# Kernel optimization log

Measured on AMD Instinct MI355X. Metric: run time of the kernel, lower is better.

## Reference

```python
import jax, jax.numpy as jnp
import numpy as np
from jax import lax

# --- config (matches init_kwargs) ---
H = 1024          # hidden_size
I = 704           # moe_intermediate_size (per expert)
E = 32            # n_routed_experts
G = 8             # n_group
TOPK_GROUP = 3    # topk_group
K = 6             # num_experts_per_tok
N_SHARED = 2      # n_shared_experts -> shared intermediate = N_SHARED * I
SCALE = 1.0       # routed_scaling_factor
T = 2048          # number of tokens
CAP = 2 * (T * K) // E


def setup_inputs() -> dict:
    key = jax.random.key(0)
    ks = jax.random.split(key, 8)
    s = 0.02  # initializer_range
    Is = N_SHARED * I
    return {
        "x": jax.random.normal(ks[0], (T, H), jnp.float32),
        "gate_w": s * jax.random.normal(ks[1], (E, H), jnp.float32),   # router
        "w_gate": s * jax.random.normal(ks[2], (E, H, I), jnp.float32),
        "w_up":   s * jax.random.normal(ks[3], (E, H, I), jnp.float32),
        "w_down": s * jax.random.normal(ks[4], (E, I, H), jnp.float32),
        "sw_gate": s * jax.random.normal(ks[5], (H, Is), jnp.float32),
        "sw_up":   s * jax.random.normal(ks[6], (H, Is), jnp.float32),
        "sw_down": s * jax.random.normal(ks[7], (Is, H), jnp.float32),
    }


def _moe_forward(x, gate_w, w_gate, w_up, w_down, sw_gate, sw_up, sw_down):
    # ---- router: softmax scores + group-limited top-k (topk_method='gready') ----
    logits = x @ gate_w.T                                  # [T, E]
    scores = jax.nn.softmax(logits, axis=-1)               # [T, E]
    group_scores = scores.reshape(T, G, E // G).max(-1)    # [T, G]
    _, gidx = lax.top_k(group_scores, TOPK_GROUP)          # [T, topk_group]
    gmask = jnp.zeros((T, G), scores.dtype).at[jnp.arange(T)[:, None], gidx].set(1.0)
    emask = jnp.repeat(gmask, E // G, axis=1)              # [T, E]
    masked_scores = jnp.where(emask > 0, scores, 0.0)
    topk_w, topk_idx = lax.top_k(masked_scores, K)         # [T, K]
    # norm_topk_prob=False -> weights are raw softmax scores * routed_scaling_factor
    topk_w = topk_w * SCALE

    # ---- dispatch: sort assignments by expert, scatter into [E, CAP, H] buffers ----
    flat_e = topk_idx.reshape(-1)                          # [T*K]
    order = jnp.argsort(flat_e)
    se = flat_e[order]                                     # sorted expert ids
    tok = order // K                                       # source token of each slot
    counts = jax.ops.segment_sum(jnp.ones_like(flat_e), flat_e, num_segments=E)
    starts = jnp.cumsum(counts) - counts
    pos = jnp.arange(T * K) - starts[se]                   # position within expert
    valid = pos < CAP
    pos_w = jnp.where(valid, pos, CAP)                     # overflow slot CAP (sliced off)
    xbuf = jnp.zeros((E, CAP + 1, H), x.dtype).at[se, pos_w].set(x[tok])
    xb = xbuf[:, :CAP]                                     # [E, CAP, H]

    # ---- grouped expert MLPs: silu(x Wg) * (x Wu) @ Wd ----
    g = jnp.einsum("ech,ehi->eci", xb, w_gate)
    u = jnp.einsum("ech,ehi->eci", xb, w_up)
    yb = jnp.einsum("eci,eih->ech", jax.nn.silu(g) * u, w_down)  # [E, CAP, H]

    # ---- combine: gather back and weighted-scatter to tokens ----
    y_flat = yb[se, jnp.minimum(pos, CAP - 1)] * valid[:, None].astype(x.dtype)
    wts = topk_w.reshape(-1)[order]                        # [T*K]
    routed = jnp.zeros((T, H), x.dtype).at[tok].add(y_flat * wts[:, None])

    # ---- shared experts MLP (intermediate = n_shared * moe_inter) ----
    sg = jax.nn.silu(x @ sw_gate) * (x @ sw_up)
    shared = sg @ sw_down

    return routed + shared                                 # [T, H]


def reference(x, gate_w, w_gate, w_up, w_down, sw_gate, sw_up, sw_down):
    return _moe_forward(x, gate_w, w_gate, w_up, w_down, sw_gate, sw_up, sw_down)
```

## Files before the change

kernel.cpp:

```cpp
#include <hip/hip_runtime.h>
#include <hip/hip_bf16.h>

#define H 1024
#define I_DIM 704
#define E 32
#define TOPK_GROUP 3
#define K_TOP 6
#define T_TOK 2048
#define CAP 768
#define IS_DIM 1408
#define NCHUNK 192

typedef __attribute__((ext_vector_type(8))) short short8v;
typedef __attribute__((ext_vector_type(4))) float f32x4;

__device__ __forceinline__ unsigned short f2bfbits(float f) {
  unsigned u = __float_as_uint(f);
  unsigned r = (u + 0x7fffu + ((u >> 16) & 1u)) >> 16;
  return (unsigned short)r;
}
__device__ __forceinline__ float bf2f(unsigned short b) {
  return __uint_as_float(((unsigned)b) << 16);
}
__device__ __forceinline__ void gload_lds16(const short* g, short* l) {
  __builtin_amdgcn_global_load_lds(
      (const __attribute__((address_space(1))) unsigned int*)g,
      (__attribute__((address_space(3))) unsigned int*)l, 16, 0, 0);
}

__global__ void cast_x_kernel(const float* __restrict__ x, short* __restrict__ xb) {
  size_t i = ((size_t)blockIdx.x * 256 + threadIdx.x) * 4;
  float4 v = *(const float4*)(x + i);
  short4 s;
  s.x = (short)f2bfbits(v.x); s.y = (short)f2bfbits(v.y);
  s.z = (short)f2bfbits(v.z); s.w = (short)f2bfbits(v.w);
  *(short4*)(xb + i) = s;
}

__global__ __launch_bounds__(256) void tw_kernel(const float* __restrict__ in,
                                                 short* __restrict__ out,
                                                 int K, int N) {
  __shared__ float tile[64][65];
  long long eoff = (long long)blockIdx.z * (long long)K * N;
  const float* ip = in + eoff;
  short* op = out + eoff;
  int n0 = blockIdx.x * 64, k0 = blockIdx.y * 64;
  int t = threadIdx.x;
  int tr = t >> 4;
  int tc = (t & 15) * 4;
  #pragma unroll
  for (int i = 0; i < 4; ++i) {
    float4 v = *(const float4*)(ip + (size_t)(k0 + tr + i * 16) * N + n0 + tc);
    tile[tr + i * 16][tc + 0] = v.x;
    tile[tr + i * 16][tc + 1] = v.y;
    tile[tr + i * 16][tc + 2] = v.z;
    tile[tr + i * 16][tc + 3] = v.w;
  }
  __syncthreads();
  #pragma unroll
  for (int i = 0; i < 4; ++i) {
    int n = tr + i * 16;
    short4 s;
    s.x = (short)f2bfbits(tile[tc + 0][n]);
    s.y = (short)f2bfbits(tile[tc + 1][n]);
    s.z = (short)f2bfbits(tile[tc + 2][n]);
    s.w = (short)f2bfbits(tile[tc + 3][n]);
    *(short4*)(op + (size_t)(n0 + n) * K + k0 + tc) = s;
  }
}

__global__ __launch_bounds__(64) void gating_kernel(const float* __restrict__ x,
                                                    const float* __restrict__ gw,
                                                    int* __restrict__ tidx,
                                                    float* __restrict__ tw) {
  int t = blockIdx.x;
  int lane = threadIdx.x;
  int e = lane & 31, half = lane >> 5;
  const float4* xr4 = (const float4*)(x + (size_t)t * H + half * 512);
  const float4* wr4 = (const float4*)(gw + (size_t)e * H + half * 512);
  double acc = 0.0;
  #pragma unroll 4
  for (int j = 0; j < 128; ++j) {
    float4 a = xr4[j], b = wr4[j];
    acc += (double)a.x * b.x + (double)a.y * b.y + (double)a.z * b.z + (double)a.w * b.w;
  }
  acc += __shfl_down(acc, 32);
  double lg = acc;
  double m = lg;
  #pragma unroll
  for (int off = 16; off >= 1; off >>= 1) {
    double o = __shfl_xor(m, off);
    if (o > m) m = o;
  }
  double p = exp(lg - m);
  double sum = p;
  #pragma unroll
  for (int off = 16; off >= 1; off >>= 1) sum += __shfl_xor(sum, off);
  p /= sum;
  double gmax = p;
  { double o = __shfl_xor(gmax, 1); if (o > gmax) gmax = o;
    o = __shfl_xor(gmax, 2); if (o > gmax) gmax = o; }
  bool gsel = false;
  double gv = gmax;
  #pragma unroll
  for (int it = 0; it < TOPK_GROUP; ++it) {
    double v = gv; int gi = e >> 2;
    #pragma unroll
    for (int off = 16; off >= 1; off >>= 1) {
      double ov = __shfl_xor(v, off);
      int oi = __shfl_xor(gi, off);
      if (ov > v || (ov == v && oi < gi)) { v = ov; gi = oi; }
    }
    if ((e >> 2) == gi) { gsel = true; gv = -1e300; }
  }
  double mp = gsel ? p : 0.0;
  #pragma unroll
  for (int it = 0; it < K_TOP; ++it) {
    double v = mp; int ei = e;
    #pragma unroll
    for (int off = 16; off >= 1; off >>= 1) {
      double ov = __shfl_xor(v, off);
      int oi = __shfl_xor(ei, off);
      if (ov > v || (ov == v && oi < ei)) { v = ov; ei = oi; }
    }
    if (lane == 0) { tidx[t * K_TOP + it] = ei; tw[t * K_TOP + it] = (float)v; }
    if (e == ei) mp = -2.0;
  }
}

__global__ __launch_bounds__(64) void hist_kernel(const int* __restrict__ tidx,
                                                  int* __restrict__ chunk_hist) {
  __shared__ int h[E];
  int c = blockIdx.x, lane = threadIdx.x;
  if (lane < E) h[lane] = 0;
  __syncthreads();
  int te = tidx[c * 64 + lane];
  atomicAdd(&h[te], 1);
  __syncthreads();
  if (lane < E) chunk_hist[c * E + lane] = h[lane];
}

__global__ __launch_bounds__(1024) void scan_kernel(const int* __restrict__ chunk_hist,
                                                    int* __restrict__ chunk_base,
                                                    int* __restrict__ cnt) {
  __shared__ int h[NCHUNK * E];
  int t = threadIdx.x;
  for (int i = t; i < NCHUNK * E; i += 1024) h[i] = chunk_hist[i];
  __syncthreads();
  if (t < E) {
    int run = 0;
    for (int c = 0; c < NCHUNK; ++c) {
      int v = h[c * E + t];
      h[c * E + t] = run;
      run += v;
    }
    cnt[t] = run < CAP ? run : CAP;
  }
  __syncthreads();
  for (int i = t; i < NCHUNK * E; i += 1024) chunk_base[i] = h[i];
}

__global__ __launch_bounds__(64) void place_kernel(const int* __restrict__ tidx,
                                                   const int* __restrict__ chunk_base,
                                                   int* __restrict__ token_list,
                                                   int* __restrict__ sid) {
  int c = blockIdx.x, lane = threadIdx.x;
  int idx = c * 64 + lane;
  int te = tidx[idx];
  unsigned long long mymask = 0;
  #pragma unroll
  for (int e = 0; e < E; ++e) {
    unsigned long long bal = __ballot(te == e);
    if (te == e) mymask = bal;
  }
  int rank = __popcll(mymask & ((1ull << lane) - 1ull));
  int pos = chunk_base[c * E + te] + rank;
  int s = -1;
  if (pos < CAP) {
    token_list[te * CAP + pos] = idx / K_TOP;
    s = te * CAP + pos;
  }
  sid[idx] = s;
}

__global__ __launch_bounds__(256) void gateup_kernel(
    const short* __restrict__ Xb, const short* __restrict__ Wg, const short* __restrict__ Wu,
    short* __restrict__ Sout, const int* __restrict__ tlist, const int* __restrict__ cnt_dev,
    int Nld, long long wstride, long long sstride) {
  int e = blockIdx.z;
  int cnt = cnt_dev ? cnt_dev[e] : T_TOK;
  int row0 = blockIdx.y * 128;
  if (row0 >= cnt) return;
  int col0 = blockIdx.x * 64;
  const short* wg = Wg + (long long)e * wstride;
  const short* wu = Wu + (long long)e * wstride;
  short* sbase = Sout + (long long)e * sstride;

  __shared__ __align__(16) short As[2][128 * 32];
  __shared__ __align__(16) short Bgs[2][64 * 32];
  __shared__ __align__(16) short Bus[2][64 * 32];

  int tid = threadIdx.x;
  int lane = tid & 63, wave = tid >> 6;

  int rr = tid >> 2, ch = tid & 3;
  int che = ch ^ ((rr >> 1) & 3);
  int ra0 = row0 + rr, ra1 = ra0 + 64;
  if (tlist) {
    const int* tl = tlist + e * CAP;
    ra0 = tl[min(ra0, cnt - 1)];
    ra1 = tl[min(ra1, cnt - 1)];
  }
  const short* pa0 = Xb + (size_t)ra0 * H + che * 8;
  const short* pa1 = Xb + (size_t)ra1 * H + che * 8;
  const short* pbg = wg + (size_t)(col0 + rr) * H + che * 8;
  const short* pbu = wu + (size_t)(col0 + rr) * H + che * 8;

  short* ldsA00 = &As[0][(wave * 16) * 32];
  short* ldsA10 = &As[0][(64 + wave * 16) * 32];
  short* ldsA01 = &As[1][(wave * 16) * 32];
  short* ldsA11 = &As[1][(64 + wave * 16) * 32];
  short* ldsBg0 = &Bgs[0][(wave * 16) * 32];
  short* ldsBg1 = &Bgs[1][(wave * 16) * 32];
  short* ldsBu0 = &Bus[0][(wave * 16) * 32];
  short* ldsBu1 = &Bus[1][(wave * 16) * 32];

  int wm = wave & 1, wn = wave >> 1;
  int c = lane & 15, q = lane >> 4;
  int qa = q ^ ((c >> 1) & 3);
  const short* fA0  = &As[0][(wm * 64 + c) * 32 + qa * 8];
  const short* fA1  = &As[1][(wm * 64 + c) * 32 + qa * 8];
  const short* fBg0 = &Bgs[0][(wn * 32 + c) * 32 + qa * 8];
  const short* fBg1 = &Bgs[1][(wn * 32 + c) * 32 + qa * 8];
  const short* fBu0 = &Bus[0][(wn * 32 + c) * 32 + qa * 8];
  const short* fBu1 = &Bus[1][(wn * 32 + c) * 32 + qa * 8];

  f32x4 accg[4][2], accu[4][2];
  #pragma unroll
  for (int i = 0; i < 4; ++i)
    #pragma unroll
    for (int j = 0; j < 2; ++j) {
      accg[i][j] = (f32x4){0.f, 0.f, 0.f, 0.f};
      accu[i][j] = (f32x4){0.f, 0.f, 0.f, 0.f};
    }

  gload_lds16(pa0, ldsA00);
  gload_lds16(pa1, ldsA10);
  gload_lds16(pbg, ldsBg0);
  gload_lds16(pbu, ldsBu0);

#define GU_PHASE(KC, FAc, FBGc, FBUc, A0d, A1d, BGd, BUd, PREF)                     \
  {                                                                                 \
    __builtin_amdgcn_s_barrier();                                                   \
    asm volatile("" ::: "memory");                                                  \
    if (PREF) {                                                                     \
      gload_lds16(pa0 + (KC) + 32, A0d);                                            \
      gload_lds16(pa1 + (KC) + 32, A1d);                                            \
      gload_lds16(pbg + (KC) + 32, BGd);                                            \
      gload_lds16(pbu + (KC) + 32, BUd);                                            \
      asm volatile("s_waitcnt vmcnt(4)" ::: "memory");                              \
    } else {                                                                        \
      asm volatile("s_waitcnt vmcnt(0)" ::: "memory");                              \
    }                                                                               \
    __builtin_amdgcn_s_barrier();                                                   \
    __builtin_amdgcn_sched_barrier(0);                                              \
    short8v a[4], bg[2], bu[2];                                                     \
    _Pragma("unroll")                                                               \
    for (int mi = 0; mi < 4; ++mi) a[mi] = *(const short8v*)((FAc) + mi * 16 * 32); \
    _Pragma("unroll")                                                               \
    for (int ni = 0; ni < 2; ++ni) {                                                \
      bg[ni] = *(const short8v*)((FBGc) + ni * 16 * 32);                            \
      bu[ni] = *(const short8v*)((FBUc) + ni * 16 * 32);                            \
    }                                                                               \
    _Pragma("unroll")                                                               \
    for (int mi = 0; mi < 4; ++mi)                                                  \
      _Pragma("unroll")                                                             \
      for (int ni = 0; ni < 2; ++ni) {                                              \
        accg[mi][ni] = __builtin_amdgcn_mfma_f32_16x16x32_bf16(a[mi], bg[ni], accg[mi][ni], 0, 0, 0); \
        accu[mi][ni] = __builtin_amdgcn_mfma_f32_16x16x32_bf16(a[mi], bu[ni], accu[mi][ni], 0, 0, 0); \
      }                                                                             \
  }

  for (int k0 = 0; k0 < H; k0 += 64) {
    GU_PHASE(k0,      fA0, fBg0, fBu0, ldsA01, ldsA11, ldsBg1, ldsBu1, true);
    GU_PHASE(k0 + 32, fA1, fBg1, fBu1, ldsA00, ldsA10, ldsBg0, ldsBu0, (k0 + 64 < H));
  }
#undef GU_PHASE

  #pragma unroll
  for (int mi = 0; mi < 4; ++mi) {
    int rbase = row0 + wm * 64 + mi * 16 + q * 4;
    #pragma unroll
    for (int ni = 0; ni < 2; ++ni) {
      int col = col0 + wn * 32 + ni * 16 + c;
      #pragma unroll
      for (int r = 0; r < 4; ++r) {
        float g = accg[mi][ni][r], u = accu[mi][ni][r];
        float s = (g / (1.f + __expf(-g))) * u;
        sbase[(size_t)(rbase + r) * Nld + col] = (short)f2bfbits(s);
      }
    }
  }
}

__global__ __launch_bounds__(256) void down_kernel(
    const short* __restrict__ Sin, const short* __restrict__ Wd,
    float* __restrict__ outF, short* __restrict__ outY,
    const int* __restrict__ cnt_dev, int Kdim, long long wstride, long long sstride) {
  int e = blockIdx.z;
  int cnt = cnt_dev ? cnt_dev[e] : T_TOK;
  int row0 = blockIdx.y * 128;
  if (row0 >= cnt) return;
  int col0 = blockIdx.x * 128;
  const short* sb = Sin + (long long)e * sstride;
  const short* wd = Wd + (long long)e * wstride;

  __shared__ __align__(16) short As[2][128 * 32];
  __shared__ __align__(16) short Bs[2][128 * 32];

  int tid = threadIdx.x;
  int lane = tid & 63, wave = tid >> 6;
  int rr = tid >> 2, ch = tid & 3;
  int che = ch ^ ((rr >> 1) & 3);

  const short* pa0 = sb + (size_t)(row0 + rr) * Kdim + che * 8;
  const short* pa1 = pa0 + (size_t)64 * Kdim;
  const short* pb0 = wd + (size_t)(col0 + rr) * Kdim + che * 8;
  const short* pb1 = pb0 + (size_t)64 * Kdim;

  short* ldsA00 = &As[0][(wave * 16) * 32];
  short* ldsA10 = &As[0][(64 + wave * 16) * 32];
  short* ldsA01 = &As[1][(wave * 16) * 32];
  short* ldsA11 = &As[1][(64 + wave * 16) * 32];
  short* ldsB00 = &Bs[0][(wave * 16) * 32];
  short* ldsB10 = &Bs[0][(64 + wave * 16) * 32];
  short* ldsB01 = &Bs[1][(wave * 16) * 32];
  short* ldsB11 = &Bs[1][(64 + wave * 16) * 32];

  int wm = wave & 1, wn = wave >> 1;
  int c = lane & 15, q = lane >> 4;
  int qa = q ^ ((c >> 1) & 3);
  const short* fA0 = &As[0][(wm * 64 + c) * 32 + qa * 8];
  const short* fA1 = &As[1][(wm * 64 + c) * 32 + qa * 8];
  const short* fB0 = &Bs[0][(wn * 64 + c) * 32 + qa * 8];
  const short* fB1 = &Bs[1][(wn * 64 + c) * 32 + qa * 8];

  f32x4 acc[4][4];
  #pragma unroll
  for (int i = 0; i < 4; ++i)
    #pragma unroll
    for (int j = 0; j < 4; ++j) acc[i][j] = (f32x4){0.f, 0.f, 0.f, 0.f};

  gload_lds16(pa0, ldsA00);
  gload_lds16(pa1, ldsA10);
  gload_lds16(pb0, ldsB00);
  gload_lds16(pb1, ldsB10);

#define DN_PHASE(KC, FAc, FBc, A0d, A1d, B0d, B1d, PREF)                            \
  {                                                                                 \
    __builtin_amdgcn_s_barrier();                                                   \
    asm volatile("" ::: "memory");                                                  \
    if (PREF) {                                                                     \
      gload_lds16(pa0 + (KC) + 32, A0d);                                            \
      gload_lds16(pa1 + (KC) + 32, A1d);                                            \
      gload_lds16(pb0 + (KC) + 32, B0d);                                            \
      gload_lds16(pb1 + (KC) + 32, B1d);                                            \
      asm volatile("s_waitcnt vmcnt(4)" ::: "memory");                              \
    } else {                                                                        \
      asm volatile("s_waitcnt vmcnt(0)" ::: "memory");                              \
    }                                                                               \
    __builtin_amdgcn_s_barrier();                                                   \
    __builtin_amdgcn_sched_barrier(0);                                              \
    short8v a[4], b[4];                                                             \
    _Pragma("unroll")                                                               \
    for (int mi = 0; mi < 4; ++mi) a[mi] = *(const short8v*)((FAc) + mi * 16 * 32); \
    _Pragma("unroll")                                                               \
    for (int ni = 0; ni < 4; ++ni) b[ni] = *(const short8v*)((FBc) + ni * 16 * 32); \
    _Pragma("unroll")                                                               \
    for (int mi = 0; mi < 4; ++mi)                                                  \
      _Pragma("unroll")                                                             \
      for (int ni = 0; ni < 4; ++ni)                                                \
        acc[mi][ni] = __builtin_amdgcn_mfma_f32_16x16x32_bf16(a[mi], b[ni], acc[mi][ni], 0, 0, 0); \
  }

  for (int k0 = 0; k0 < Kdim; k0 += 64) {
    DN_PHASE(k0,      fA0, fB0, ldsA01, ldsA11, ldsB01, ldsB11, true);
    DN_PHASE(k0 + 32, fA1, fB1, ldsA00, ldsA10, ldsB00, ldsB10, (k0 + 64 < Kdim));
  }
#undef DN_PHASE

  if (outY) {
    #pragma unroll
    for (int mi = 0; mi < 4; ++mi) {
      int rb = row0 + wm * 64 + mi * 16 + q * 4;
      #pragma unroll
      for (int r = 0; r < 4; ++r) {
        short* yrow = outY + (size_t)(e * CAP + rb + r) * H;
        #pragma unroll
        for (int ni = 0; ni < 4; ++ni) {
          int col = col0 + wn * 64 + ni * 16 + c;
          yrow[col] = (short)f2bfbits(acc[mi][ni][r]);
        }
      }
    }
  } else {
    #pragma unroll
    for (int mi = 0; mi < 4; ++mi) {
      int rb = row0 + wm * 64 + mi * 16 + q * 4;
      #pragma unroll
      for (int ni = 0; ni < 4; ++ni) {
        int col = col0 + wn * 64 + ni * 16 + c;
        #pragma unroll
        for (int r = 0; r < 4; ++r)
          outF[(size_t)(rb + r) * H + col] = acc[mi][ni][r];
      }
    }
  }
}

__global__ __launch_bounds__(256) void combine_kernel(
    const short* __restrict__ Yr, const int* __restrict__ sid,
    const float* __restrict__ twt, float* __restrict__ out) {
  int t = blockIdx.x;
  int col = threadIdx.x * 4;
  float* op = out + (size_t)t * H + col;
  float4 o = *(float4*)op;
  #pragma unroll
  for (int k = 0; k < K_TOP; ++k) {
    int s = sid[t * K_TOP + k];
    if (s >= 0) {
      float w = twt[t * K_TOP + k];
      ushort4 y = *(const ushort4*)(Yr + (size_t)s * H + col);
      o.x += w * bf2f(y.x);
      o.y += w * bf2f(y.y);
      o.z += w * bf2f(y.z);
      o.w += w * bf2f(y.w);
    }
  }
  *(float4*)op = o;
}

extern "C" void kernel_launch(void* const* d_in, const int* in_sizes, int n_in,
                              void* d_out, int out_size, void* d_ws, size_t ws_size,
                              hipStream_t stream) {
  const float* x       = (const float*)d_in[0];
  const float* gate_w  = (const float*)d_in[1];
  const float* w_gate  = (const float*)d_in[2];
  const float* w_up    = (const float*)d_in[3];
  const float* w_down  = (const float*)d_in[4];
  const float* sw_gate = (const float*)d_in[5];
  const float* sw_up   = (const float*)d_in[6];
  const float* sw_down = (const float*)d_in[7];
  float* out = (float*)d_out;
  char* ws = (char*)d_ws;

  size_t o = 0;
  short* xb   = (short*)(ws + o); o += (size_t)T_TOK * H * 2;
  short* Sr   = (short*)(ws + o); o += (size_t)E * CAP * I_DIM * 2;
  short* Ss   = (short*)(ws + o); o += (size_t)T_TOK * IS_DIM * 2;
  short* wg_t = (short*)(ws + o);
  short* Yr   = (short*)(ws + o); o += (size_t)E * H * I_DIM * 2;
  short* wu_t = (short*)(ws + o); o += (size_t)E * H * I_DIM * 2;
  short* wd_t = (short*)(ws + o); o += (size_t)E * I_DIM * H * 2;
  short* swg_t = (short*)(ws + o); o += (size_t)H * IS_DIM * 2;
  short* swu_t = (short*)(ws + o); o += (size_t)H * IS_DIM * 2;
  short* swd_t = (short*)(ws + o); o += (size_t)IS_DIM * H * 2;
  int*   tidx = (int*)(ws + o);   o += (size_t)T_TOK * K_TOP * 4;
  float* twt  = (float*)(ws + o); o += (size_t)T_TOK * K_TOP * 4;
  int*   sid  = (int*)(ws + o);   o += (size_t)T_TOK * K_TOP * 4;
  int*   tl   = (int*)(ws + o);   o += (size_t)E * CAP * 4;
  int*   cnt  = (int*)(ws + o);   o += 256;
  int*   chist = (int*)(ws + o);  o += (size_t)NCHUNK * E * 4;
  int*   cbase = (int*)(ws + o);  o += (size_t)NCHUNK * E * 4;

  cast_x_kernel<<<(T_TOK * H) / 1024, 256, 0, stream>>>(x, xb);
  gating_kernel<<<T_TOK, 64, 0, stream>>>(x, gate_w, tidx, twt);
  hist_kernel<<<NCHUNK, 64, 0, stream>>>(tidx, chist);
  scan_kernel<<<1, 1024, 0, stream>>>(chist, cbase, cnt);
  place_kernel<<<NCHUNK, 64, 0, stream>>>(tidx, cbase, tl, sid);

  tw_kernel<<<dim3(I_DIM / 64, H / 64, E), 256, 0, stream>>>(w_gate, wg_t, H, I_DIM);
  tw_kernel<<<dim3(I_DIM / 64, H / 64, E), 256, 0, stream>>>(w_up,   wu_t, H, I_DIM);
  tw_kernel<<<dim3(H / 64, I_DIM / 64, E), 256, 0, stream>>>(w_down, wd_t, I_DIM, H);
  tw_kernel<<<dim3(IS_DIM / 64, H / 64, 1), 256, 0, stream>>>(sw_gate, swg_t, H, IS_DIM);
  tw_kernel<<<dim3(IS_DIM / 64, H / 64, 1), 256, 0, stream>>>(sw_up,   swu_t, H, IS_DIM);
  tw_kernel<<<dim3(H / 64, IS_DIM / 64, 1), 256, 0, stream>>>(sw_down, swd_t, IS_DIM, H);

  gateup_kernel<<<dim3(I_DIM / 64, CAP / 128, E), 256, 0, stream>>>(
      xb, wg_t, wu_t, Sr, tl, cnt, I_DIM, (long long)H * I_DIM, (long long)CAP * I_DIM);
  gateup_kernel<<<dim3(IS_DIM / 64, T_TOK / 128, 1), 256, 0, stream>>>(
      xb, swg_t, swu_t, Ss, nullptr, nullptr, IS_DIM, 0, 0);
  down_kernel<<<dim3(H / 128, T_TOK / 128, 1), 256, 0, stream>>>(
      Ss, swd_t, out, nullptr, nullptr, IS_DIM, 0, 0);
  down_kernel<<<dim3(H / 128, CAP / 128, E), 256, 0, stream>>>(
      Sr, wd_t, nullptr, Yr, cnt, I_DIM, (long long)I_DIM * H, (long long)CAP * I_DIM);
  combine_kernel<<<T_TOK, 256, 0, stream>>>(Yr, sid, twt, out);
}
```

Before: 548.3 us.

## Triple-buffer LDS pipeline, remap blocks across XCDs, raise MFMA priority

```diff
diff --git a/kernel.cpp b/kernel.cpp
--- a/kernel.cpp
+++ b/kernel.cpp
@@ -187,18 +187,31 @@
     const short* __restrict__ Xb, const short* __restrict__ Wg, const short* __restrict__ Wu,
     short* __restrict__ Sout, const int* __restrict__ tlist, const int* __restrict__ cnt_dev,
     int Nld, long long wstride, long long sstride) {
-  int e = blockIdx.z;
+  int bx = blockIdx.x, by = blockIdx.y, bz = blockIdx.z;
+  if (tlist) {
+    int gx = gridDim.x, gy = gridDim.y;
+    int total = gx * gy * gridDim.z;
+    int cpx = total >> 3;
+    int lin = bx + gx * (by + gy * bz);
+    int lin2 = (lin & 7) * cpx + (lin >> 3);
+    int pe = gx * gy;
+    bz = lin2 / pe;
+    int r = lin2 % pe;
+    by = r % gy;
+    bx = r / gy;
+  }
+  int e = bz;
   int cnt = cnt_dev ? cnt_dev[e] : T_TOK;
-  int row0 = blockIdx.y * 128;
+  int row0 = by * 128;
   if (row0 >= cnt) return;
-  int col0 = blockIdx.x * 64;
+  int col0 = bx * 64;
   const short* wg = Wg + (long long)e * wstride;
   const short* wu = Wu + (long long)e * wstride;
   short* sbase = Sout + (long long)e * sstride;
 
-  __shared__ __align__(16) short As[2][128 * 32];
-  __shared__ __align__(16) short Bgs[2][64 * 32];
-  __shared__ __align__(16) short Bus[2][64 * 32];
+  __shared__ __align__(16) short As[3][128 * 32];
+  __shared__ __align__(16) short Bgs[3][64 * 32];
+  __shared__ __align__(16) short Bus[3][64 * 32];
 
   int tid = threadIdx.x;
   int lane = tid & 63, wave = tid >> 6;
@@ -216,24 +229,9 @@
   const short* pbg = wg + (size_t)(col0 + rr) * H + che * 8;
   const short* pbu = wu + (size_t)(col0 + rr) * H + che * 8;
 
-  short* ldsA00 = &As[0][(wave * 16) * 32];
-  short* ldsA10 = &As[0][(64 + wave * 16) * 32];
-  short* ldsA01 = &As[1][(wave * 16) * 32];
-  short* ldsA11 = &As[1][(64 + wave * 16) * 32];
-  short* ldsBg0 = &Bgs[0][(wave * 16) * 32];
-  short* ldsBg1 = &Bgs[1][(wave * 16) * 32];
-  short* ldsBu0 = &Bus[0][(wave * 16) * 32];
-  short* ldsBu1 = &Bus[1][(wave * 16) * 32];
-
   int wm = wave & 1, wn = wave >> 1;
   int c = lane & 15, q = lane >> 4;
   int qa = q ^ ((c >> 1) & 3);
-  const short* fA0  = &As[0][(wm * 64 + c) * 32 + qa * 8];
-  const short* fA1  = &As[1][(wm * 64 + c) * 32 + qa * 8];
-  const short* fBg0 = &Bgs[0][(wn * 32 + c) * 32 + qa * 8];
-  const short* fBg1 = &Bgs[1][(wn * 32 + c) * 32 + qa * 8];
-  const short* fBu0 = &Bus[0][(wn * 32 + c) * 32 + qa * 8];
-  const short* fBu1 = &Bus[1][(wn * 32 + c) * 32 + qa * 8];
 
   f32x4 accg[4][2], accu[4][2];
   #pragma unroll
@@ -244,48 +242,54 @@
       accu[i][j] = (f32x4){0.f, 0.f, 0.f, 0.f};
     }
 
-  gload_lds16(pa0, ldsA00);
-  gload_lds16(pa1, ldsA10);
-  gload_lds16(pbg, ldsBg0);
-  gload_lds16(pbu, ldsBu0);
-
-#define GU_PHASE(KC, FAc, FBGc, FBUc, A0d, A1d, BGd, BUd, PREF)                     \
-  {                                                                                 \
-    __builtin_amdgcn_s_barrier();                                                   \
-    asm volatile("" ::: "memory");                                                  \
-    if (PREF) {                                                                     \
-      gload_lds16(pa0 + (KC) + 32, A0d);                                            \
-      gload_lds16(pa1 + (KC) + 32, A1d);                                            \
-      gload_lds16(pbg + (KC) + 32, BGd);                                            \
-      gload_lds16(pbu + (KC) + 32, BUd);                                            \
-      asm volatile("s_waitcnt vmcnt(4)" ::: "memory");                              \
-    } else {                                                                        \
-      asm volatile("s_waitcnt vmcnt(0)" ::: "memory");                              \
-    }                                                                               \
-    __builtin_amdgcn_s_barrier();                                                   \
-    __builtin_amdgcn_sched_barrier(0);                                              \
-    short8v a[4], bg[2], bu[2];                                                     \
-    _Pragma("unroll")                                                               \
-    for (int mi = 0; mi < 4; ++mi) a[mi] = *(const short8v*)((FAc) + mi * 16 * 32); \
-    _Pragma("unroll")                                                               \
-    for (int ni = 0; ni < 2; ++ni) {                                                \
-      bg[ni] = *(const short8v*)((FBGc) + ni * 16 * 32);                            \
-      bu[ni] = *(const short8v*)((FBUc) + ni * 16 * 32);                            \
-    }                                                                               \
-    _Pragma("unroll")                                                               \
-    for (int mi = 0; mi < 4; ++mi)                                                  \
-      _Pragma("unroll")                                                             \
-      for (int ni = 0; ni < 2; ++ni) {                                              \
+#define STAGE_GU(KK, B)                                       \
+  gload_lds16(pa0 + (KK), &As[B][(wave * 16) * 32]);          \
+  gload_lds16(pa1 + (KK), &As[B][(64 + wave * 16) * 32]);     \
+  gload_lds16(pbg + (KK), &Bgs[B][(wave * 16) * 32]);         \
+  gload_lds16(pbu + (KK), &Bus[B][(wave * 16) * 32]);
+
+  STAGE_GU(0, 0)
+  STAGE_GU(32, 1)
+
+#define GU_PHASE(KC, B, NB)                                                          \
+  {                                                                                  \
+    __builtin_amdgcn_s_barrier();                                                    \
+    asm volatile("" ::: "memory");                                                   \
+    { int kk = (KC) + 64; if (kk >= H) kk = 0;                                       \
+      STAGE_GU(kk, NB) }                                                             \
+    asm volatile("s_waitcnt vmcnt(8)" ::: "memory");                                 \
+    __builtin_amdgcn_s_barrier();                                                    \
+    __builtin_amdgcn_sched_barrier(0);                                               \
+    short8v a[4], bg[2], bu[2];                                                      \
+    _Pragma("unroll")                                                                \
+    for (int mi = 0; mi < 4; ++mi)                                                   \
+      a[mi] = *(const short8v*)(&As[B][(wm * 64 + mi * 16 + c) * 32 + qa * 8]);      \
+    _Pragma("unroll")                                                                \
+    for (int ni = 0; ni < 2; ++ni) {                                                 \
+      bg[ni] = *(const short8v*)(&Bgs[B][(wn * 32 + ni * 16 + c) * 32 + qa * 8]);    \
+      bu[ni] = *(const short8v*)(&Bus[B][(wn * 32 + ni * 16 + c) * 32 + qa * 8]);    \
+    }                                                                                \
+    __builtin_amdgcn_s_setprio(1);                                                   \
+    _Pragma("unroll")                                                                \
+    for (int mi = 0; mi < 4; ++mi)                                                   \
+      _Pragma("unroll")                                                              \
+      for (int ni = 0; ni < 2; ++ni) {                                               \
         accg[mi][ni] = __builtin_amdgcn_mfma_f32_16x16x32_bf16(a[mi], bg[ni], accg[mi][ni], 0, 0, 0); \
         accu[mi][ni] = __builtin_amdgcn_mfma_f32_16x16x32_bf16(a[mi], bu[ni], accu[mi][ni], 0, 0, 0); \
-      }                                                                             \
-  }
-
-  for (int k0 = 0; k0 < H; k0 += 64) {
-    GU_PHASE(k0,      fA0, fBg0, fBu0, ldsA01, ldsA11, ldsBg1, ldsBu1, true);
-    GU_PHASE(k0 + 32, fA1, fBg1, fBu1, ldsA00, ldsA10, ldsBg0, ldsBu0, (k0 + 64 < H));
-  }
+      }                                                                              \
+    __builtin_amdgcn_s_setprio(0);                                                   \
+  }
+
+  for (int k0 = 0; k0 < 960; k0 += 96) {
+    GU_PHASE(k0, 0, 2)
+    GU_PHASE(k0 + 32, 1, 0)
+    GU_PHASE(k0 + 64, 2, 1)
+  }
+  GU_PHASE(960, 0, 2)
+  GU_PHASE(992, 1, 0)
 #undef GU_PHASE
+#undef STAGE_GU
+  asm volatile("s_waitcnt vmcnt(0)" ::: "memory");
 
   #pragma unroll
   for (int mi = 0; mi < 4; ++mi) {
@@ -307,16 +311,29 @@
     const short* __restrict__ Sin, const short* __restrict__ Wd,
     float* __restrict__ outF, short* __restrict__ outY,
     const int* __restrict__ cnt_dev, int Kdim, long long wstride, long long sstride) {
-  int e = blockIdx.z;
+  int bx = blockIdx.x, by = blockIdx.y, bz = blockIdx.z;
+  if (cnt_dev) {
+    int gx = gridDim.x, gy = gridDim.y;
+    int total = gx * gy * gridDim.z;
+    int cpx = total >> 3;
+    int lin = bx + gx * (by + gy * bz);
+    int lin2 = (lin & 7) * cpx + (lin >> 3);
+    int pe = gx * gy;
+    bz = lin2 / pe;
+    int r = lin2 % pe;
+    by = r % gy;
+    bx = r / gy;
+  }
+  int e = bz;
   int cnt = cnt_dev ? cnt_dev[e] : T_TOK;
-  int row0 = blockIdx.y * 128;
+  int row0 = by * 128;
   if (row0 >= cnt) return;
-  int col0 = blockIdx.x * 128;
+  int col0 = bx * 128;
   const short* sb = Sin + (long long)e * sstride;
   const short* wd = Wd + (long long)e * wstride;
 
-  __shared__ __align__(16) short As[2][128 * 32];
-  __shared__ __align__(16) short Bs[2][128 * 32];
+  __shared__ __align__(16) short As[3][128 * 32];
+  __shared__ __align__(16) short Bs[3][128 * 32];
 
   int tid = threadIdx.x;
   int lane = tid & 63, wave = tid >> 6;
@@ -328,22 +345,9 @@
   const short* pb0 = wd + (size_t)(col0 + rr) * Kdim + che * 8;
   const short* pb1 = pb0 + (size_t)64 * Kdim;
 
-  short* ldsA00 = &As[0][(wave * 16) * 32];
-  short* ldsA10 = &As[0][(64 + wave * 16) * 32];
-  short* ldsA01 = &As[1][(wave * 16) * 32];
-  short* ldsA11 = &As[1][(64 + wave * 16) * 32];
-  short* ldsB00 = &Bs[0][(wave * 16) * 32];
-  short* ldsB10 = &Bs[0][(64 + wave * 16) * 32];
-  short* ldsB01 = &Bs[1][(wave * 16) * 32];
-  short* ldsB11 = &Bs[1][(64 + wave * 16) * 32];
-
   int wm = wave & 1, wn = wave >> 1;
   int c = lane & 15, q = lane >> 4;
   int qa = q ^ ((c >> 1) & 3);
-  const short* fA0 = &As[0][(wm * 64 + c) * 32 + qa * 8];
-  const short* fA1 = &As[1][(wm * 64 + c) * 32 + qa * 8];
-  const short* fB0 = &Bs[0][(wn * 64 + c) * 32 + qa * 8];
-  const short* fB1 = &Bs[1][(wn * 64 + c) * 32 + qa * 8];
 
   f32x4 acc[4][4];
   #pragma unroll
@@ -351,43 +355,56 @@
     #pragma unroll
     for (int j = 0; j < 4; ++j) acc[i][j] = (f32x4){0.f, 0.f, 0.f, 0.f};
 
-  gload_lds16(pa0, ldsA00);
-  gload_lds16(pa1, ldsA10);
-  gload_lds16(pb0, ldsB00);
-  gload_lds16(pb1, ldsB10);
-
-#define DN_PHASE(KC, FAc, FBc, A0d, A1d, B0d, B1d, PREF)                            \
-  {                                                                                 \
-    __builtin_amdgcn_s_barrier();                                                   \
-    asm volatile("" ::: "memory");                                                  \
-    if (PREF) {                                                                     \
-      gload_lds16(pa0 + (KC) + 32, A0d);                                            \
-      gload_lds16(pa1 + (KC) + 32, A1d);                                            \
-      gload_lds16(pb0 + (KC) + 32, B0d);                                            \
-      gload_lds16(pb1 + (KC) + 32, B1d);                                            \
-      asm volatile("s_waitcnt vmcnt(4)" ::: "memory");                              \
-    } else {                                                                        \
-      asm volatile("s_waitcnt vmcnt(0)" ::: "memory");                              \
-    }                                                                               \
-    __builtin_amdgcn_s_barrier();                                                   \
-    __builtin_amdgcn_sched_barrier(0);                                              \
-    short8v a[4], b[4];                                                             \
-    _Pragma("unroll")                                                               \
-    for (int mi = 0; mi < 4; ++mi) a[mi] = *(const short8v*)((FAc) + mi * 16 * 32); \
-    _Pragma("unroll")                                                               \
-    for (int ni = 0; ni < 4; ++ni) b[ni] = *(const short8v*)((FBc) + ni * 16 * 32); \
-    _Pragma("unroll")                                                               \
-    for (int mi = 0; mi < 4; ++mi)                                                  \
-      _Pragma("unroll")                                                             \
-      for (int ni = 0; ni < 4; ++ni)                                                \
+#define STAGE_DN(KK, B)                                       \
+  gload_lds16(pa0 + (KK), &As[B][(wave * 16) * 32]);          \
+  gload_lds16(pa1 + (KK), &As[B][(64 + wave * 16) * 32]);     \
+  gload_lds16(pb0 + (KK), &Bs[B][(wave * 16) * 32]);          \
+  gload_lds16(pb1 + (KK), &Bs[B][(64 + wave * 16) * 32]);
+
+  STAGE_DN(0, 0)
+  STAGE_DN(32, 1)
+
+#define DN_PHASE(KC, B, NB)                                                          \
+  {                                                                                  \
+    __builtin_amdgcn_s_barrier();                                                    \
+    asm volatile("" ::: "memory");                                                   \
+    { int kk = (KC) + 64; if (kk >= Kdim) kk = 0;                                    \
+      STAGE_DN(kk, NB) }                                                             \
+    asm volatile("s_waitcnt vmcnt(8)" ::: "memory");                                 \
+    __builtin_amdgcn_s_barrier();                                                    \
+    __builtin_amdgcn_sched_barrier(0);                                               \
+    short8v a[4], b[4];                                                              \
+    _Pragma("unroll")                                                                \
+    for (int mi = 0; mi < 4; ++mi)                                                   \
+      a[mi] = *(const short8v*)(&As[B][(wm * 64 + mi * 16 + c) * 32 + qa * 8]);      \
+    _Pragma("unroll")                                                                \
+    for (int ni = 0; ni < 4; ++ni)                                                   \
+      b[ni] = *(const short8v*)(&Bs[B][(wn * 64 + ni * 16 + c) * 32 + qa * 8]);      \
+    __builtin_amdgcn_s_setprio(1);                                                   \
+    _Pragma("unroll")                                                                \
+    for (int mi = 0; mi < 4; ++mi)                                                   \
+      _Pragma("unroll")                                                              \
+      for (int ni = 0; ni < 4; ++ni)                                                 \
         acc[mi][ni] = __builtin_amdgcn_mfma_f32_16x16x32_bf16(a[mi], b[ni], acc[mi][ni], 0, 0, 0); \
-  }
-
-  for (int k0 = 0; k0 < Kdim; k0 += 64) {
-    DN_PHASE(k0,      fA0, fB0, ldsA01, ldsA11, ldsB01, ldsB11, true);
-    DN_PHASE(k0 + 32, fA1, fB1, ldsA00, ldsA10, ldsB00, ldsB10, (k0 + 64 < Kdim));
+    __builtin_amdgcn_s_setprio(0);                                                   \
+  }
+
+  {
+    int nph = Kdim >> 5;
+    int ntr = nph / 3;
+    int tail = nph - ntr * 3;
+    int k0 = 0;
+    for (int t3 = 0; t3 < ntr; ++t3, k0 += 96) {
+      DN_PHASE(k0, 0, 2)
+      DN_PHASE(k0 + 32, 1, 0)
+      DN_PHASE(k0 + 64, 2, 1)
+    }
+    if (tail >= 1) { DN_PHASE(k0, 0, 2) }
+    if (tail >= 2) { DN_PHASE(k0 + 32, 1, 0) }
   }
 #undef DN_PHASE
+#undef STAGE_DN
+  asm volatile("s_waitcnt vmcnt(0)" ::: "memory");
 
   if (outY) {
     #pragma unroll
```

New measurement: 539.4 us. About the same (-1.6%).
